# Kernel tuning notes

Measured on AMD Instinct MI355X. Metric: run time of the kernel, lower is better.

Reference implementation:

```python
import jax, jax.numpy as jnp
import numpy as np

B, D, K = 32768, 1024, 64
N3, N4, N5 = 512, 512, 512


def setup_inputs() -> dict:
    key = jax.random.key(0)
    ks = jax.random.split(key, 10)
    # x in [-1, 1]^D as the docstring states
    x = jax.random.uniform(ks[0], (B, D), dtype=jnp.float32, minval=-1.0, maxval=1.0)
    S = jnp.sort(jax.random.randint(ks[1], (K,), 0, D, dtype=jnp.int32))
    a = jax.random.normal(ks[2], (K,), dtype=jnp.float32)
    b = jax.random.normal(ks[3], (K, K), dtype=jnp.float32)
    idx3 = jax.random.randint(ks[4], (N3, 3), 0, K, dtype=jnp.int32)
    c3 = jax.random.normal(ks[5], (N3,), dtype=jnp.float32)
    idx4 = jax.random.randint(ks[6], (N4, 4), 0, K, dtype=jnp.int32)
    c4 = jax.random.normal(ks[7], (N4,), dtype=jnp.float32)
    idx5 = jax.random.randint(ks[8], (N5, 5), 0, K, dtype=jnp.int32)
    c5 = jax.random.normal(ks[9], (N5,), dtype=jnp.float32)
    return {"x": x, "S": S, "a": a, "b": b, "idx3": idx3, "c3": c3,
            "idx4": idx4, "c4": c4, "idx5": idx5, "c5": c5}


def _monomial_term(xS, idx, c):
    # xS: (B,k); idx: (n,deg); c: (n,) -> (B,)
    # gather -> (B, n, deg), product over monomial factors, weighted sum
    prod = jnp.prod(xS[:, idx], axis=2)  # (B, n)
    return prod @ c


def reference(x, S, a, b, idx3, c3, idx4, c4, idx5, c5):
    xS = x[:, S]                      # (B, k)
    lin = xS @ a                      # (B,)
    # sum_{i<j} b[i,j] xS_i xS_j == einsum with strictly-upper-triangular b
    bu = jnp.triu(b, k=1)             # (k, k)
    quad = jnp.einsum('bi,ij,bj->b', xS, bu, xS)
    out = lin + quad
    out = out + _monomial_term(xS, idx3, c3)
    out = out + _monomial_term(xS, idx4, c4)
    out = out + _monomial_term(xS, idx5, c5)
    return out
```

## Files before the change

### kernel.cpp

```cpp
#include <hip/hip_runtime.h>
#include <stdint.h>

#define NT 256
#define RPB 64
#define XSTR_B 272

#define WS_BU   0
#define WS_P3   16384
#define WS_P4   24576
#define WS_C4   32768
#define WS_P5   34816
#define WS_P5B  43008

static __device__ __forceinline__ float4 f4fma(float s, float4 v, float4 acc) {
    acc.x += s * v.x; acc.y += s * v.y; acc.z += s * v.z; acc.w += s * v.w;
    return acc;
}

__global__ void prepack_kernel(const float* __restrict__ b,
                               const int* __restrict__ i3, const float* __restrict__ c3,
                               const int* __restrict__ i4, const float* __restrict__ c4,
                               const int* __restrict__ i5, const float* __restrict__ c5,
                               unsigned char* __restrict__ ws)
{
    const int g = blockIdx.x * NT + threadIdx.x;
    const int stride = gridDim.x * NT;
    float* bu  = (float*)(ws + WS_BU);
    uint4* p3  = (uint4*)(ws + WS_P3);
    uint4* p4  = (uint4*)(ws + WS_P4);
    float* c4o = (float*)(ws + WS_C4);
    uint4* p5  = (uint4*)(ws + WS_P5);
    uint2* p5b = (uint2*)(ws + WS_P5B);

    for (int e = g; e < 4096; e += stride) {
        int i = e >> 6, j = e & 63;
        bu[e] = (i < j) ? b[e] : 0.0f;
    }
    for (int t = g; t < 512; t += stride) {
        p3[t] = make_uint4((unsigned)i3[3*t+0] * XSTR_B, (unsigned)i3[3*t+1] * XSTR_B,
                           (unsigned)i3[3*t+2] * XSTR_B, __float_as_uint(c3[t]));
        p4[t] = make_uint4((unsigned)i4[4*t+0] * XSTR_B, (unsigned)i4[4*t+1] * XSTR_B,
                           (unsigned)i4[4*t+2] * XSTR_B, (unsigned)i4[4*t+3] * XSTR_B);
        c4o[t] = c4[t];
        p5[t] = make_uint4((unsigned)i5[5*t+0] * XSTR_B, (unsigned)i5[5*t+1] * XSTR_B,
                           (unsigned)i5[5*t+2] * XSTR_B, (unsigned)i5[5*t+3] * XSTR_B);
        p5b[t] = make_uint2((unsigned)i5[5*t+4] * XSTR_B, __float_as_uint(c5[t]));
    }
}

__global__ __launch_bounds__(NT, 2)
void poly_main(const float* __restrict__ x, const int* __restrict__ S,
               const float* __restrict__ a,
               const unsigned char* __restrict__ ws,
               float* __restrict__ out)
{
    __shared__ float xS[64 * 68];
    __shared__ float bS[64 * 64];
    __shared__ float aS[64];
    __shared__ short slot[1024];
    __shared__ short lead[64];
    __shared__ float red[1024];

    const int tid  = threadIdx.x;
    const int row0 = blockIdx.x * RPB;

    ((short4*)slot)[tid] = make_short4(-1, -1, -1, -1);
    {
        const float4* bin = (const float4*)(ws + WS_BU);
        float4* bsh = (float4*)bS;
        #pragma unroll
        for (int m = 0; m < 4; ++m) bsh[tid + m * NT] = bin[tid + m * NT];
    }
    if (tid < 64) aS[tid] = a[tid];
    __syncthreads();
    if (tid < 64) {
        int sv = S[tid];
        int k0 = tid;
        while (k0 > 0 && S[k0 - 1] == sv) --k0;
        lead[tid] = (short)k0;
        if (k0 == tid) slot[sv] = (short)tid;
    }
    __syncthreads();

    {
        short4 sl = ((short4*)slot)[tid];
        int o0 = (int)sl.x * XSTR_B;
        int o1 = (int)sl.y * XSTR_B;
        int o2 = (int)sl.z * XSTR_B;
        int o3 = (int)sl.w * XSTR_B;
        const float4* Xrow = (const float4*)(x + (size_t)row0 * 1024);
        char* xsb = (char*)xS;
        #pragma unroll 4
        for (int r = 0; r < RPB; ++r) {
            float4 v = Xrow[r * 256 + tid];
            int rb = r * 4;
            if (sl.x >= 0) *(float*)(xsb + o0 + rb) = v.x;
            if (sl.y >= 0) *(float*)(xsb + o1 + rb) = v.y;
            if (sl.z >= 0) *(float*)(xsb + o2 + rb) = v.z;
            if (sl.w >= 0) *(float*)(xsb + o3 + rb) = v.w;
        }
    }
    __syncthreads();

    {
        int k = tid >> 2, q = tid & 3;
        int k0 = lead[k];
        if (k0 != k) {
            float4* dst = (float4*)((char*)xS + k  * XSTR_B) + q * 4;
            const float4* src = (const float4*)((char*)xS + k0 * XSTR_B) + q * 4;
            #pragma unroll
            for (int m = 0; m < 4; ++m) dst[m] = src[m];
        }
    }
    __syncthreads();

    const int rg = tid & 15;
    const int ts = tid >> 4;
    const char* xb = (const char*)xS + rg * 16;

    float4 d0 = make_float4(0.f, 0.f, 0.f, 0.f);
    float4 d1 = d0, d2 = d0, d3 = d0;
    #pragma unroll 8
    for (int i = 0; i < 64; ++i) {
        float4 xi = *(const float4*)(xb + i * XSTR_B);
        float b0 = bS[i * 64 + ts];
        float b1 = bS[i * 64 + ts + 16];
        float b2 = bS[i * 64 + ts + 32];
        float b3 = bS[i * 64 + ts + 48];
        d0 = f4fma(b0, xi, d0);
        d1 = f4fma(b1, xi, d1);
        d2 = f4fma(b2, xi, d2);
        d3 = f4fma(b3, xi, d3);
    }
    float4 xj0 = *(const float4*)(xb + (ts +  0) * XSTR_B);
    float4 xj1 = *(const float4*)(xb + (ts + 16) * XSTR_B);
    float4 xj2 = *(const float4*)(xb + (ts + 32) * XSTR_B);
    float4 xj3 = *(const float4*)(xb + (ts + 48) * XSTR_B);
    float a0 = aS[ts], a1 = aS[ts + 16], a2 = aS[ts + 32], a3 = aS[ts + 48];

    float4 acc;
    acc.x = (a0 + d0.x) * xj0.x + (a1 + d1.x) * xj1.x + (a2 + d2.x) * xj2.x + (a3 + d3.x) * xj3.x;
    acc.y = (a0 + d0.y) * xj0.y + (a1 + d1.y) * xj1.y + (a2 + d2.y) * xj2.y + (a3 + d3.y) * xj3.y;
    acc.z = (a0 + d0.z) * xj0.z + (a1 + d1.z) * xj1.z + (a2 + d2.z) * xj2.z + (a3 + d3.z) * xj3.z;
    acc.w = (a0 + d0.w) * xj0.w + (a1 + d1.w) * xj1.w + (a2 + d2.w) * xj2.w + (a3 + d3.w) * xj3.w;

    const uint4* p3g  = (const uint4*)(ws + WS_P3);
    const uint4* p4g  = (const uint4*)(ws + WS_P4);
    const float* c4g  = (const float*)(ws + WS_C4);
    const uint4* p5g  = (const uint4*)(ws + WS_P5);
    const uint2* p5bg = (const uint2*)(ws + WS_P5B);

    #pragma unroll 2
    for (int m = 0; m < 32; ++m) {
        uint4 p = p3g[16 * m + ts];
        float4 v0 = *(const float4*)(xb + p.x);
        float4 v1 = *(const float4*)(xb + p.y);
        float4 v2 = *(const float4*)(xb + p.z);
        float c = __uint_as_float(p.w);
        acc.x += c * (v0.x * v1.x * v2.x);
        acc.y += c * (v0.y * v1.y * v2.y);
        acc.z += c * (v0.z * v1.z * v2.z);
        acc.w += c * (v0.w * v1.w * v2.w);
    }
    #pragma unroll 2
    for (int m = 0; m < 32; ++m) {
        uint4 p = p4g[16 * m + ts];
        float c = c4g[16 * m + ts];
        float4 v0 = *(const float4*)(xb + p.x);
        float4 v1 = *(const float4*)(xb + p.y);
        float4 v2 = *(const float4*)(xb + p.z);
        float4 v3 = *(const float4*)(xb + p.w);
        acc.x += c * ((v0.x * v1.x) * (v2.x * v3.x));
        acc.y += c * ((v0.y * v1.y) * (v2.y * v3.y));
        acc.z += c * ((v0.z * v1.z) * (v2.z * v3.z));
        acc.w += c * ((v0.w * v1.w) * (v2.w * v3.w));
    }
    #pragma unroll 2
    for (int m = 0; m < 32; ++m) {
        uint4 p = p5g[16 * m + ts];
        uint2 q = p5bg[16 * m + ts];
        float4 v0 = *(const float4*)(xb + p.x);
        float4 v1 = *(const float4*)(xb + p.y);
        float4 v2 = *(const float4*)(xb + p.z);
        float4 v3 = *(const float4*)(xb + p.w);
        float4 v4 = *(const float4*)(xb + q.x);
        float c = __uint_as_float(q.y);
        acc.x += c * (((v0.x * v1.x) * (v2.x * v3.x)) * v4.x);
        acc.y += c * (((v0.y * v1.y) * (v2.y * v3.y)) * v4.y);
        acc.z += c * (((v0.z * v1.z) * (v2.z * v3.z)) * v4.z);
        acc.w += c * (((v0.w * v1.w) * (v2.w * v3.w)) * v4.w);
    }

    ((float4*)red)[ts * 16 + rg] = acc;
    __syncthreads();
    if (tid < 64) {
        float s = 0.f;
        #pragma unroll
        for (int t = 0; t < 16; ++t) s += red[t * 64 + tid];
        out[row0 + tid] = s;
    }
}

extern "C" void kernel_launch(void* const* d_in, const int* in_sizes, int n_in,
                              void* d_out, int out_size, void* d_ws, size_t ws_size,
                              hipStream_t stream) {
    const float* x  = (const float*)d_in[0];
    const int*   S  = (const int*)d_in[1];
    const float* a  = (const float*)d_in[2];
    const float* b  = (const float*)d_in[3];
    const int*   i3 = (const int*)d_in[4];
    const float* c3 = (const float*)d_in[5];
    const int*   i4 = (const int*)d_in[6];
    const float* c4 = (const float*)d_in[7];
    const int*   i5 = (const int*)d_in[8];
    const float* c5 = (const float*)d_in[9];
    unsigned char* ws = (unsigned char*)d_ws;
    float* out = (float*)d_out;

    prepack_kernel<<<16, NT, 0, stream>>>(b, i3, c3, i4, c4, i5, c5, ws);
    poly_main<<<32768 / RPB, NT, 0, stream>>>(x, S, a, ws, out);
}
```

Measured before the change: 236.8 us.

## Restructure poly kernel: 16 rows per block, column-group gather, bf16 coeffs, shuffle reduce

Cuts rows per block from 64 to 16 and raises the occupancy target. Moves the S-to-slot mapping into the prepack kernel, so each block loads only the 16-byte column groups that hold selected columns, not whole 4KB rows. Monomial index tables are packed as 16-bit offsets with bf16 coefficients and staged into shared memory. The quadratic term now walks a transposed triangular b from global memory and skips the zero part. The final reduction uses wave shuffles instead of a large shared buffer. Rounding coefficients to bf16 loses precision and may exceed tolerance.

```diff
diff --git a/kernel.cpp b/kernel.cpp
--- a/kernel.cpp
+++ b/kernel.cpp
@@ -2,170 +2,199 @@
 #include <stdint.h>
 
 #define NT 256
-#define RPB 64
-#define XSTR_B 272
-
-#define WS_BU   0
-#define WS_P3   16384
-#define WS_P4   24576
-#define WS_C4   32768
-#define WS_P5   34816
-#define WS_P5B  43008
-
+#define RPB 16
+#define XSTR 80
+
+#define WS_TAB   0
+#define TB_P3    0
+#define TB_P4    4096
+#define TB_P5    8192
+#define TB_P5E   12288
+#define TB_C4    13312
+#define TB_C5    14336
+#define TB_SZ    15360
+#define WS_BUT   15360
+#define WS_CGCOL 31744
+#define WS_CGSL  32000
+#define WS_LEAD  32512
+
+static __device__ __forceinline__ unsigned short f2bf(float f) {
+    unsigned u = __float_as_uint(f);
+    return (unsigned short)((u + 0x7FFFu + ((u >> 16) & 1u)) >> 16);
+}
+static __device__ __forceinline__ float bf2f(unsigned short h) {
+    return __uint_as_float((unsigned)h << 16);
+}
 static __device__ __forceinline__ float4 f4fma(float s, float4 v, float4 acc) {
     acc.x += s * v.x; acc.y += s * v.y; acc.z += s * v.z; acc.w += s * v.w;
     return acc;
 }
 
-__global__ void prepack_kernel(const float* __restrict__ b,
-                               const int* __restrict__ i3, const float* __restrict__ c3,
-                               const int* __restrict__ i4, const float* __restrict__ c4,
-                               const int* __restrict__ i5, const float* __restrict__ c5,
-                               unsigned char* __restrict__ ws)
+__global__ void prepack(const int* __restrict__ S, const float* __restrict__ b,
+                        const int* __restrict__ i3, const float* __restrict__ c3,
+                        const int* __restrict__ i4, const float* __restrict__ c4,
+                        const int* __restrict__ i5, const float* __restrict__ c5,
+                        unsigned char* __restrict__ ws)
 {
-    const int g = blockIdx.x * NT + threadIdx.x;
-    const int stride = gridDim.x * NT;
-    float* bu  = (float*)(ws + WS_BU);
-    uint4* p3  = (uint4*)(ws + WS_P3);
-    uint4* p4  = (uint4*)(ws + WS_P4);
-    float* c4o = (float*)(ws + WS_C4);
-    uint4* p5  = (uint4*)(ws + WS_P5);
-    uint2* p5b = (uint2*)(ws + WS_P5B);
-
-    for (int e = g; e < 4096; e += stride) {
-        int i = e >> 6, j = e & 63;
-        bu[e] = (i < j) ? b[e] : 0.0f;
-    }
-    for (int t = g; t < 512; t += stride) {
-        p3[t] = make_uint4((unsigned)i3[3*t+0] * XSTR_B, (unsigned)i3[3*t+1] * XSTR_B,
-                           (unsigned)i3[3*t+2] * XSTR_B, __float_as_uint(c3[t]));
-        p4[t] = make_uint4((unsigned)i4[4*t+0] * XSTR_B, (unsigned)i4[4*t+1] * XSTR_B,
-                           (unsigned)i4[4*t+2] * XSTR_B, (unsigned)i4[4*t+3] * XSTR_B);
-        c4o[t] = c4[t];
-        p5[t] = make_uint4((unsigned)i5[5*t+0] * XSTR_B, (unsigned)i5[5*t+1] * XSTR_B,
-                           (unsigned)i5[5*t+2] * XSTR_B, (unsigned)i5[5*t+3] * XSTR_B);
-        p5b[t] = make_uint2((unsigned)i5[5*t+4] * XSTR_B, __float_as_uint(c5[t]));
-    }
-}
-
-__global__ __launch_bounds__(NT, 2)
-void poly_main(const float* __restrict__ x, const int* __restrict__ S,
-               const float* __restrict__ a,
-               const unsigned char* __restrict__ ws,
-               float* __restrict__ out)
-{
-    __shared__ float xS[64 * 68];
-    __shared__ float bS[64 * 64];
-    __shared__ float aS[64];
-    __shared__ short slot[1024];
-    __shared__ short lead[64];
-    __shared__ float red[1024];
-
-    const int tid  = threadIdx.x;
-    const int row0 = blockIdx.x * RPB;
-
-    ((short4*)slot)[tid] = make_short4(-1, -1, -1, -1);
-    {
-        const float4* bin = (const float4*)(ws + WS_BU);
-        float4* bsh = (float4*)bS;
-        #pragma unroll
-        for (int m = 0; m < 4; ++m) bsh[tid + m * NT] = bin[tid + m * NT];
-    }
-    if (tid < 64) aS[tid] = a[tid];
+    __shared__ short slotS[1024];
+    __shared__ int cnt;
+    const int tid = threadIdx.x;
+    for (int e = tid; e < 1024; e += NT) slotS[e] = -1;
+    if (tid == 0) cnt = 0;
     __syncthreads();
     if (tid < 64) {
         int sv = S[tid];
         int k0 = tid;
         while (k0 > 0 && S[k0 - 1] == sv) --k0;
-        lead[tid] = (short)k0;
-        if (k0 == tid) slot[sv] = (short)tid;
-    }
-    __syncthreads();
-
-    {
-        short4 sl = ((short4*)slot)[tid];
-        int o0 = (int)sl.x * XSTR_B;
-        int o1 = (int)sl.y * XSTR_B;
-        int o2 = (int)sl.z * XSTR_B;
-        int o3 = (int)sl.w * XSTR_B;
-        const float4* Xrow = (const float4*)(x + (size_t)row0 * 1024);
-        char* xsb = (char*)xS;
+        ((short*)(ws + WS_LEAD))[tid] = (short)k0;
+        if (k0 == tid) slotS[sv] = (short)tid;
+    }
+    __syncthreads();
+    int* cgcol = (int*)(ws + WS_CGCOL);
+    short4* cgsl = (short4*)(ws + WS_CGSL);
+    {
+        int g = tid;
+        short s0 = slotS[4*g], s1 = slotS[4*g+1], s2 = slotS[4*g+2], s3 = slotS[4*g+3];
+        if (s0 >= 0 || s1 >= 0 || s2 >= 0 || s3 >= 0) {
+            int pos = atomicAdd(&cnt, 1);
+            cgcol[pos] = g;
+            cgsl[pos] = make_short4(s0 >= 0 ? (short)(s0 * XSTR) : (short)-1,
+                                    s1 >= 0 ? (short)(s1 * XSTR) : (short)-1,
+                                    s2 >= 0 ? (short)(s2 * XSTR) : (short)-1,
+                                    s3 >= 0 ? (short)(s3 * XSTR) : (short)-1);
+        }
+    }
+    __syncthreads();
+    if (tid == 0) {
+        for (int p = cnt; p < 64; ++p) {
+            cgcol[p] = 0;
+            cgsl[p] = make_short4(-1, -1, -1, -1);
+        }
+    }
+    float* buT = (float*)(ws + WS_BUT);
+    for (int e = tid; e < 4096; e += NT) {
+        int j = e >> 6, i = e & 63;
+        buT[e] = (i < j) ? b[i * 64 + j] : 0.0f;
+    }
+    ushort4* p3 = (ushort4*)(ws + TB_P3);
+    ushort4* p4 = (ushort4*)(ws + TB_P4);
+    ushort4* p5 = (ushort4*)(ws + TB_P5);
+    unsigned short* p5e = (unsigned short*)(ws + TB_P5E);
+    unsigned short* c4h = (unsigned short*)(ws + TB_C4);
+    unsigned short* c5h = (unsigned short*)(ws + TB_C5);
+    for (int t = tid; t < 512; t += NT) {
+        p3[t] = make_ushort4((unsigned short)(i3[3*t+0]*XSTR), (unsigned short)(i3[3*t+1]*XSTR),
+                             (unsigned short)(i3[3*t+2]*XSTR), f2bf(c3[t]));
+        p4[t] = make_ushort4((unsigned short)(i4[4*t+0]*XSTR), (unsigned short)(i4[4*t+1]*XSTR),
+                             (unsigned short)(i4[4*t+2]*XSTR), (unsigned short)(i4[4*t+3]*XSTR));
+        p5[t] = make_ushort4((unsigned short)(i5[5*t+0]*XSTR), (unsigned short)(i5[5*t+1]*XSTR),
+                             (unsigned short)(i5[5*t+2]*XSTR), (unsigned short)(i5[5*t+3]*XSTR));
+        p5e[t] = (unsigned short)(i5[5*t+4]*XSTR);
+        c4h[t] = f2bf(c4[t]);
+        c5h[t] = f2bf(c5[t]);
+    }
+}
+
+__global__ __launch_bounds__(NT, 6)
+void poly_main(const float* __restrict__ x, const float* __restrict__ a,
+               const unsigned char* __restrict__ ws, float* __restrict__ out)
+{
+    __shared__ float xS[64 * 20];
+    __shared__ unsigned char tabL[TB_SZ];
+    __shared__ float red[64];
+
+    const int tid  = threadIdx.x;
+    const int row0 = blockIdx.x * RPB;
+
+    {
+        const uint4* src = (const uint4*)(ws + WS_TAB);
+        uint4* dst = (uint4*)tabL;
+        for (int e = tid; e < TB_SZ / 16; e += NT) dst[e] = src[e];
+    }
+    {
+        const int g = tid & 63, rs = tid >> 6;
+        int col4 = ((const int*)(ws + WS_CGCOL))[g];
+        short4 sl = ((const short4*)(ws + WS_CGSL))[g];
+        if (sl.x >= 0 || sl.y >= 0 || sl.z >= 0 || sl.w >= 0) {
+            const float4* Xrow = (const float4*)(x + (size_t)row0 * 1024);
+            char* xsb = (char*)xS;
+            #pragma unroll
+            for (int m = 0; m < 4; ++m) {
+                int r = rs * 4 + m;
+                float4 v = Xrow[r * 256 + col4];
+                int rb = r * 4;
+                if (sl.x >= 0) *(float*)(xsb + sl.x + rb) = v.x;
+                if (sl.y >= 0) *(float*)(xsb + sl.y + rb) = v.y;
+                if (sl.z >= 0) *(float*)(xsb + sl.z + rb) = v.z;
+                if (sl.w >= 0) *(float*)(xsb + sl.w + rb) = v.w;
+            }
+        }
+    }
+    __syncthreads();
+    {
+        int k = tid >> 2, q = tid & 3;
+        int k0 = ((const short*)(ws + WS_LEAD))[k];
+        if (k0 != k) {
+            float4* dst = (float4*)((char*)xS + k  * XSTR);
+            const float4* src = (const float4*)((char*)xS + k0 * XSTR);
+            dst[q] = src[q];
+        }
+    }
+    __syncthreads();
+
+    const int rg = tid & 3;
+    const int ts = tid >> 2;
+    const char* xb = (const char*)xS + rg * 16;
+
+    float4 d = make_float4(0.f, 0.f, 0.f, 0.f);
+    {
+        const float4* buT4 = (const float4*)(ws + WS_BUT) + ts * 16;
+        const int nii = (ts + 3) >> 2;
         #pragma unroll 4
-        for (int r = 0; r < RPB; ++r) {
-            float4 v = Xrow[r * 256 + tid];
-            int rb = r * 4;
-            if (sl.x >= 0) *(float*)(xsb + o0 + rb) = v.x;
-            if (sl.y >= 0) *(float*)(xsb + o1 + rb) = v.y;
-            if (sl.z >= 0) *(float*)(xsb + o2 + rb) = v.z;
-            if (sl.w >= 0) *(float*)(xsb + o3 + rb) = v.w;
-        }
-    }
-    __syncthreads();
-
-    {
-        int k = tid >> 2, q = tid & 3;
-        int k0 = lead[k];
-        if (k0 != k) {
-            float4* dst = (float4*)((char*)xS + k  * XSTR_B) + q * 4;
-            const float4* src = (const float4*)((char*)xS + k0 * XSTR_B) + q * 4;
-            #pragma unroll
-            for (int m = 0; m < 4; ++m) dst[m] = src[m];
-        }
-    }
-    __syncthreads();
-
-    const int rg = tid & 15;
-    const int ts = tid >> 4;
-    const char* xb = (const char*)xS + rg * 16;
-
-    float4 d0 = make_float4(0.f, 0.f, 0.f, 0.f);
-    float4 d1 = d0, d2 = d0, d3 = d0;
-    #pragma unroll 8
-    for (int i = 0; i < 64; ++i) {
-        float4 xi = *(const float4*)(xb + i * XSTR_B);
-        float b0 = bS[i * 64 + ts];
-        float b1 = bS[i * 64 + ts + 16];
-        float b2 = bS[i * 64 + ts + 32];
-        float b3 = bS[i * 64 + ts + 48];
-        d0 = f4fma(b0, xi, d0);
-        d1 = f4fma(b1, xi, d1);
-        d2 = f4fma(b2, xi, d2);
-        d3 = f4fma(b3, xi, d3);
-    }
-    float4 xj0 = *(const float4*)(xb + (ts +  0) * XSTR_B);
-    float4 xj1 = *(const float4*)(xb + (ts + 16) * XSTR_B);
-    float4 xj2 = *(const float4*)(xb + (ts + 32) * XSTR_B);
-    float4 xj3 = *(const float4*)(xb + (ts + 48) * XSTR_B);
-    float a0 = aS[ts], a1 = aS[ts + 16], a2 = aS[ts + 32], a3 = aS[ts + 48];
-
+        for (int ii = 0; ii < nii; ++ii) {
+            float4 bb  = buT4[ii];
+            float4 xi0 = *(const float4*)(xb + (ii * 4 + 0) * XSTR);
+            float4 xi1 = *(const float4*)(xb + (ii * 4 + 1) * XSTR);
+            float4 xi2 = *(const float4*)(xb + (ii * 4 + 2) * XSTR);
+            float4 xi3 = *(const float4*)(xb + (ii * 4 + 3) * XSTR);
+            d = f4fma(bb.x, xi0, d);
+            d = f4fma(bb.y, xi1, d);
+            d = f4fma(bb.z, xi2, d);
+            d = f4fma(bb.w, xi3, d);
+        }
+    }
+    float av = a[ts];
+    float4 xj = *(const float4*)(xb + ts * XSTR);
     float4 acc;
-    acc.x = (a0 + d0.x) * xj0.x + (a1 + d1.x) * xj1.x + (a2 + d2.x) * xj2.x + (a3 + d3.x) * xj3.x;
-    acc.y = (a0 + d0.y) * xj0.y + (a1 + d1.y) * xj1.y + (a2 + d2.y) * xj2.y + (a3 + d3.y) * xj3.y;
-    acc.z = (a0 + d0.z) * xj0.z + (a1 + d1.z) * xj1.z + (a2 + d2.z) * xj2.z + (a3 + d3.z) * xj3.z;
-    acc.w = (a0 + d0.w) * xj0.w + (a1 + d1.w) * xj1.w + (a2 + d2.w) * xj2.w + (a3 + d3.w) * xj3.w;
-
-    const uint4* p3g  = (const uint4*)(ws + WS_P3);
-    const uint4* p4g  = (const uint4*)(ws + WS_P4);
-    const float* c4g  = (const float*)(ws + WS_C4);
-    const uint4* p5g  = (const uint4*)(ws + WS_P5);
-    const uint2* p5bg = (const uint2*)(ws + WS_P5B);
-
-    #pragma unroll 2
-    for (int m = 0; m < 32; ++m) {
-        uint4 p = p3g[16 * m + ts];
+    acc.x = (av + d.x) * xj.x;
+    acc.y = (av + d.y) * xj.y;
+    acc.z = (av + d.z) * xj.z;
+    acc.w = (av + d.w) * xj.w;
+
+    const ushort4* p3L = (const ushort4*)(tabL + TB_P3);
+    const ushort4* p4L = (const ushort4*)(tabL + TB_P4);
+    const ushort4* p5L = (const ushort4*)(tabL + TB_P5);
+    const unsigned short* p5eL = (const unsigned short*)(tabL + TB_P5E);
+    const unsigned short* c4L  = (const unsigned short*)(tabL + TB_C4);
+    const unsigned short* c5L  = (const unsigned short*)(tabL + TB_C5);
+
+    #pragma unroll 4
+    for (int m = 0; m < 8; ++m) {
+        ushort4 p = p3L[64 * m + ts];
         float4 v0 = *(const float4*)(xb + p.x);
         float4 v1 = *(const float4*)(xb + p.y);
         float4 v2 = *(const float4*)(xb + p.z);
-        float c = __uint_as_float(p.w);
-        acc.x += c * (v0.x * v1.x * v2.x);
-        acc.y += c * (v0.y * v1.y * v2.y);
-        acc.z += c * (v0.z * v1.z * v2.z);
-        acc.w += c * (v0.w * v1.w * v2.w);
+        float c = bf2f(p.w);
+        acc.x += c * ((v0.x * v1.x) * v2.x);
+        acc.y += c * ((v0.y * v1.y) * v2.y);
+        acc.z += c * ((v0.z * v1.z) * v2.z);
+        acc.w += c * ((v0.w * v1.w) * v2.w);
     }
     #pragma unroll 2
-    for (int m = 0; m < 32; ++m) {
-        uint4 p = p4g[16 * m + ts];
-        float c = c4g[16 * m + ts];
+    for (int m = 0; m < 8; ++m) {
+        int t = 64 * m + ts;
+        ushort4 p = p4L[t];
+        float c = bf2f(c4L[t]);
         float4 v0 = *(const float4*)(xb + p.x);
         float4 v1 = *(const float4*)(xb + p.y);
         float4 v2 = *(const float4*)(xb + p.z);
@@ -176,27 +205,35 @@
         acc.w += c * ((v0.w * v1.w) * (v2.w * v3.w));
     }
     #pragma unroll 2
-    for (int m = 0; m < 32; ++m) {
-        uint4 p = p5g[16 * m + ts];
-        uint2 q = p5bg[16 * m + ts];
+    for (int m = 0; m < 8; ++m) {
+        int t = 64 * m + ts;
+        ushort4 p = p5L[t];
+        int o4 = p5eL[t];
+        float c = bf2f(c5L[t]);
         float4 v0 = *(const float4*)(xb + p.x);
         float4 v1 = *(const float4*)(xb + p.y);
         float4 v2 = *(const float4*)(xb + p.z);
         float4 v3 = *(const float4*)(xb + p.w);
-        float4 v4 = *(const float4*)(xb + q.x);
-        float c = __uint_as_float(q.y);
+        float4 v4 = *(const float4*)(xb + o4);
         acc.x += c * (((v0.x * v1.x) * (v2.x * v3.x)) * v4.x);
         acc.y += c * (((v0.y * v1.y) * (v2.y * v3.y)) * v4.y);
         acc.z += c * (((v0.z * v1.z) * (v2.z * v3.z)) * v4.z);
         acc.w += c * (((v0.w * v1.w) * (v2.w * v3.w)) * v4.w);
     }
 
-    ((float4*)red)[ts * 16 + rg] = acc;
-    __syncthreads();
-    if (tid < 64) {
-        float s = 0.f;
-        #pragma unroll
-        for (int t = 0; t < 16; ++t) s += red[t * 64 + tid];
+    #pragma unroll
+    for (int mask = 4; mask <= 32; mask <<= 1) {
+        acc.x += __shfl_xor(acc.x, mask, 64);
+        acc.y += __shfl_xor(acc.y, mask, 64);
+        acc.z += __shfl_xor(acc.z, mask, 64);
+        acc.w += __shfl_xor(acc.w, mask, 64);
+    }
+    const int w = tid >> 6;
+    const int lane = tid & 63;
+    if (lane < 4) ((float4*)red)[w * 4 + lane] = acc;
+    __syncthreads();
+    if (tid < 16) {
+        float s = red[tid] + red[16 + tid] + red[32 + tid] + red[48 + tid];
         out[row0 + tid] = s;
     }
 }
@@ -217,6 +254,6 @@
     unsigned char* ws = (unsigned char*)d_ws;
     float* out = (float*)d_out;
 
-    prepack_kernel<<<16, NT, 0, stream>>>(b, i3, c3, i4, c4, i5, c5, ws);
-    poly_main<<<32768 / RPB, NT, 0, stream>>>(x, S, a, ws, out);
-}
+    prepack<<<1, NT, 0, stream>>>(S, b, i3, c3, i4, c4, i5, c5, ws);
+    poly_main<<<32768 / RPB, NT, 0, stream>>>(x, a, ws, out);
+}
```

Measured after the change: 230.9 us. 2.5% less time.
